# Optimization experiments

Measured on AMD Instinct MI355X. Metric: run time of the kernel, lower is better.

The kernel has to match this reference:

```python
import jax, jax.numpy as jnp
import numpy as np

D_MODEL = 1024
NUM_HEADS = 16
D_HEAD = D_MODEL // NUM_HEADS
NEG_INF = float(np.finfo(np.float32).min)


def setup_inputs() -> dict:
    key = jax.random.key(0)
    ks = jax.random.split(key, 6)
    B, S = 2, 2048
    q = jax.random.normal(ks[0], (B, S, D_MODEL), dtype=jnp.float32)
    k = jax.random.normal(ks[1], (B, S, D_MODEL), dtype=jnp.float32)
    v = jax.random.normal(ks[2], (B, S, D_MODEL), dtype=jnp.float32)
    # causal boolean mask: True = attend
    attn_mask = jnp.tril(jnp.ones((S, S), dtype=bool))
    # nn.Linear(d_model, d_model, bias=False) weights: [out, in]; y = x @ W.T
    init_scale = 1.0 / np.sqrt(D_MODEL)
    Wq = jax.random.uniform(ks[3], (D_MODEL, D_MODEL), jnp.float32, -init_scale, init_scale)
    Wk = jax.random.uniform(ks[4], (D_MODEL, D_MODEL), jnp.float32, -init_scale, init_scale)
    Wv = jax.random.uniform(ks[5], (D_MODEL, D_MODEL), jnp.float32, -init_scale, init_scale)
    return {"query": q, "key": k, "value": v, "Wq": Wq, "Wk": Wk, "Wv": Wv,
            "attn_mask": attn_mask}


def _split_heads(x):
    # [B, S, D_MODEL] -> [B, H, S, d_head]
    B, S, _ = x.shape
    return x.reshape(B, S, NUM_HEADS, D_HEAD).transpose(0, 2, 1, 3)


def reference(query, key, value, Wq, Wk, Wv, attn_mask):
    B, Sq, _ = query.shape
    Sk = key.shape[1]
    q = _split_heads(query @ Wq.T)   # [B, H, Sq, dh]
    k = _split_heads(key @ Wk.T)     # [B, H, Sk, dh]
    v = _split_heads(value @ Wv.T)   # [B, H, Sk, dh]
    scale = 1.0 / np.sqrt(D_HEAD)
    scores = jnp.einsum('bhqd,bhkd->bhqk', q, k) * scale  # [B, H, Sq, Sk]
    scores = jnp.where(attn_mask[None, None, :, :], scores, NEG_INF)
    attn_weights = jax.nn.softmax(scores, axis=-1)
    ctx = jnp.einsum('bhqk,bhkd->bhqd', attn_weights, v)   # [B, H, Sq, dh]
    context = ctx.transpose(0, 2, 1, 3).reshape(B, Sq, D_MODEL)
    return context, attn_weights
```

## Files before the change

kernel.cpp:

```cpp
#include <hip/hip_runtime.h>
#include <hip/hip_bf16.h>

#define B_ 2
#define H_ 16
#define S_ 2048
#define DH_ 64
#define DM_ 1024
#define BH_ (B_*H_)
#define CTX_ELEMS (B_*S_*DM_)
#define HEAD_ELEMS (S_*DH_)

typedef __attribute__((ext_vector_type(4))) float  f32x4;
typedef __attribute__((ext_vector_type(8))) short  short8;
typedef __attribute__((ext_vector_type(4))) unsigned short ush4;
typedef unsigned short u16;
typedef unsigned int u32;

__device__ __forceinline__ u16 f2bf(float f) {
  union { __hip_bfloat16 h; u16 u; } cv;
  cv.h = __float2bfloat16(f);
  return cv.u;
}
__device__ __forceinline__ float bf2f(u16 u) {
  union { unsigned int i; float f; } cv;
  cv.i = ((unsigned int)u) << 16;
  return cv.f;
}

__device__ __forceinline__ void gload_lds16(const u16* g, u16* l) {
  __builtin_amdgcn_global_load_lds(
      (const __attribute__((address_space(1))) u32*)g,
      (__attribute__((address_space(3))) u32*)l, 16, 0, 0);
}

__global__ __launch_bounds__(256) void convert_w(
    const float* __restrict__ w0, const float* __restrict__ w1,
    const float* __restrict__ w2, u16* __restrict__ o)
{
  const float* s = (blockIdx.y == 0) ? w0 : (blockIdx.y == 1) ? w1 : w2;
  u16* d = o + (size_t)blockIdx.y * (DM_ * DM_);
  const int i = (blockIdx.x * 256 + threadIdx.x) * 8;
  f32x4 a = *(const f32x4*)(s + i);
  f32x4 b = *(const f32x4*)(s + i + 4);
  short8 p;
#pragma unroll
  for (int j = 0; j < 4; ++j) { p[j] = (short)f2bf(a[j]); p[4 + j] = (short)f2bf(b[j]); }
  *(short8*)(d + i) = p;
}

__global__ __launch_bounds__(256) void proj_gemm(
    const float* __restrict__ X0, const float* __restrict__ X1, const float* __restrict__ X2,
    const u16* __restrict__ Wb,
    u16* __restrict__ O0, u16* __restrict__ O1, u16* __restrict__ O2)
{
  const float* X; u16* O;
  if (blockIdx.z == 0)      { X = X0; O = O0; }
  else if (blockIdx.z == 1) { X = X1; O = O1; }
  else                      { X = X2; O = O2; }
  const u16* W = Wb + (size_t)blockIdx.z * (DM_ * DM_);

  const int m0 = blockIdx.x * 128;
  const int n0 = blockIdx.y * 128;

  __shared__ u16 As[128][40];
  __shared__ u16 Bs[128 * 32];

  const int tid  = threadIdx.x;
  const int lane = tid & 63;
  const int w    = tid >> 6;
  const int wr   = w >> 1, wc = w & 1;
  const int l15  = lane & 15, l4 = lane >> 4;

  f32x4 acc[4][4];
#pragma unroll
  for (int i = 0; i < 4; ++i)
#pragma unroll
    for (int j = 0; j < 4; ++j) acc[i][j] = (f32x4){0.f, 0.f, 0.f, 0.f};

  const int srow  = tid >> 1;
  const int skoff = (tid & 1) * 16;

  const int brow0 = (w * 2) * 16 + (lane >> 2);
  const int bkoff = (lane & 3) * 8;

  for (int kb = 0; kb < DM_ / 32; ++kb) {
    const int k0 = kb * 32;
    gload_lds16(W + (size_t)(n0 + brow0) * DM_ + k0 + bkoff, &Bs[(w * 2) * 512]);
    gload_lds16(W + (size_t)(n0 + brow0 + 16) * DM_ + k0 + bkoff, &Bs[(w * 2 + 1) * 512]);
    {
      const float* ap = X + (size_t)(m0 + srow) * DM_ + k0 + skoff;
      float xa[16];
      *(f32x4*)&xa[0]  = *(const f32x4*)(ap);
      *(f32x4*)&xa[4]  = *(const f32x4*)(ap + 4);
      *(f32x4*)&xa[8]  = *(const f32x4*)(ap + 8);
      *(f32x4*)&xa[12] = *(const f32x4*)(ap + 12);
      short8 pa0, pa1;
#pragma unroll
      for (int j = 0; j < 8; ++j) {
        pa0[j] = (short)f2bf(xa[j]);
        pa1[j] = (short)f2bf(xa[8 + j]);
      }
      *(short8*)&As[srow][skoff]     = pa0;
      *(short8*)&As[srow][skoff + 8] = pa1;
    }
    __syncthreads();
    short8 af[4], bfr[4];
#pragma unroll
    for (int i = 0; i < 4; ++i)
      af[i] = *(const short8*)&As[wr * 64 + i * 16 + l15][l4 * 8];
#pragma unroll
    for (int j = 0; j < 4; ++j)
      bfr[j] = *(const short8*)&Bs[(wc * 64 + j * 16 + l15) * 32 + l4 * 8];
#pragma unroll
    for (int i = 0; i < 4; ++i)
#pragma unroll
      for (int j = 0; j < 4; ++j)
        acc[i][j] = __builtin_amdgcn_mfma_f32_16x16x32_bf16(af[i], bfr[j], acc[i][j], 0, 0, 0);
    __syncthreads();
  }

#pragma unroll
  for (int i = 0; i < 4; ++i) {
#pragma unroll
    for (int j = 0; j < 4; ++j) {
#pragma unroll
      for (int r = 0; r < 4; ++r) {
        const int grow = m0 + wr * 64 + i * 16 + l4 * 4 + r;
        const int gcol = n0 + wc * 64 + j * 16 + l15;
        const int b = grow >> 11, s = grow & (S_ - 1);
        const int h = gcol >> 6,  d = gcol & (DH_ - 1);
        O[(size_t)((b << 4) + h) * HEAD_ELEMS + (size_t)s * DH_ + d] = f2bf(acc[i][j][r]);
      }
    }
  }
}

__global__ __launch_bounds__(256) void transpose_v(const u16* __restrict__ vb,
                                                   u16* __restrict__ vt)
{
  __shared__ u16 T[64][72];
  const int bh = blockIdx.y;
  const int s0 = blockIdx.x * 64;
  const int tid = threadIdx.x;
  {
    const int sl = tid >> 2, dof = (tid & 3) * 16;
    const u16* src = vb + (size_t)bh * HEAD_ELEMS + (size_t)(s0 + sl) * DH_ + dof;
    *(short8*)&T[sl][dof]     = *(const short8*)(src);
    *(short8*)&T[sl][dof + 8] = *(const short8*)(src + 8);
  }
  __syncthreads();
  {
    const int dd = tid >> 2, sof = (tid & 3) * 16;
    u16* dst = vt + (size_t)bh * HEAD_ELEMS + (size_t)dd * S_ + s0 + sof;
    short8 t0, t1;
#pragma unroll
    for (int j = 0; j < 8; ++j) t0[j] = (short)T[sof + j][dd];
#pragma unroll
    for (int j = 0; j < 8; ++j) t1[j] = (short)T[sof + 8 + j][dd];
    *(short8*)(dst)     = t0;
    *(short8*)(dst + 8) = t1;
  }
}

#define PROW 2048
#define ATT_SMEM (16 * PROW * 2 + 16 * 4 + 64 * 4)

__global__ __launch_bounds__(256) void attn_kernel(
    const u16* __restrict__ qb, const u16* __restrict__ kb, const u16* __restrict__ vt,
    float* __restrict__ ctx, float* __restrict__ attnw)
{
  extern __shared__ u16 smem[];
  u16* P = smem;
  float* rinv    = (float*)(smem + 16 * PROW);
  float* partial = rinv + 16;

  const int bh = blockIdx.y;
  const int qt = 127 - blockIdx.x;
  const int tid = threadIdx.x;
  const int lane = tid & 63;
  const int w = tid >> 6;
  const int l15 = lane & 15, l4 = lane >> 4;

  const int NCC = ((qt * 16 + 16) + 127) >> 7;
  const int ncols = NCC << 7;

  const u16* Qb = qb + (size_t)bh * HEAD_ELEMS + (size_t)(qt * 16) * DH_;
  const u16* Kb = kb + (size_t)bh * HEAD_ELEMS;
  const u16* Vt = vt + (size_t)bh * HEAD_ELEMS;

  {
    short8 aQ0 = *(const short8*)(Qb + (size_t)l15 * DH_ + l4 * 8);
    short8 aQ1 = *(const short8*)(Qb + (size_t)l15 * DH_ + l4 * 8 + 32);
    const int qrow = l4 * 4;
    const int qabs = qt * 16 + qrow;
    float psum[4] = {0.f, 0.f, 0.f, 0.f};
    for (int ci = 0; ci < NCC; ++ci) {
      const int col0 = (ci << 7) + w * 32;
#pragma unroll
      for (int t = 0; t < 2; ++t) {
        const int ct = col0 + t * 16;
        const u16* kp = Kb + (size_t)(ct + l15) * DH_ + l4 * 8;
        short8 b0 = *(const short8*)(kp);
        short8 b1 = *(const short8*)(kp + 32);
        f32x4 a = (f32x4){0.f, 0.f, 0.f, 0.f};
        a = __builtin_amdgcn_mfma_f32_16x16x32_bf16(aQ0, b0, a, 0, 0, 0);
        a = __builtin_amdgcn_mfma_f32_16x16x32_bf16(aQ1, b1, a, 0, 0, 0);
        const int cg = ct + l15;
#pragma unroll
        for (int r = 0; r < 4; ++r) {
          const float e = (cg <= qabs + r) ? __expf(a[r] * 0.125f) : 0.f;
          psum[r] += e;
          const int row = qrow + r;
          P[(row << 11) + (cg ^ ((row & 7) << 3))] = f2bf(e);
        }
      }
    }
#pragma unroll
    for (int r = 0; r < 4; ++r) {
      float s = psum[r];
      s += __shfl_xor(s, 1);
      s += __shfl_xor(s, 2);
      s += __shfl_xor(s, 4);
      s += __shfl_xor(s, 8);
      if (l15 == 0) partial[w * 16 + qrow + r] = s;
    }
  }
  __syncthreads();
  if (tid < 16) {
    const float l = partial[tid] + partial[16 + tid] + partial[32 + tid] + partial[48 + tid];
    rinv[tid] = 1.0f / l;
  }
  __syncthreads();

  {
    const int row = tid >> 4, sub = tid & 15;
    const float inv = rinv[row];
    const int swz = (row & 7) << 3;
    const u16* prow = P + (row << 11);
    float* orow = attnw + (size_t)bh * ((size_t)S_ * S_) + (size_t)(qt * 16 + row) * S_;
    for (int c4 = sub * 4; c4 < S_; c4 += 64) {
      f32x4 o;
      if (c4 < ncols) {
        ush4 pv = *(const ush4*)(prow + (c4 ^ swz));
        o[0] = bf2f(pv[0]) * inv;
        o[1] = bf2f(pv[1]) * inv;
        o[2] = bf2f(pv[2]) * inv;
        o[3] = bf2f(pv[3]) * inv;
      } else {
        o = (f32x4){0.f, 0.f, 0.f, 0.f};
      }
      __builtin_nontemporal_store(o, (f32x4*)(orow + c4));
    }
  }

  {
    const int dq = w;
    f32x4 acc = (f32x4){0.f, 0.f, 0.f, 0.f};
    const u16* vp0 = Vt + (size_t)(dq * 16 + l15) * S_ + l4 * 8;
    const u16* prow = P + (l15 << 11);
    const int swz = (l15 & 7) << 3;
#pragma unroll 2
    for (int c = 0; c < ncols; c += 32) {
      short8 ap = *(const short8*)(prow + ((c + l4 * 8) ^ swz));
      short8 bv = *(const short8*)(vp0 + c);
      acc = __builtin_amdgcn_mfma_f32_16x16x32_bf16(ap, bv, acc, 0, 0, 0);
    }
    const int b = bh >> 4, h = bh & 15;
#pragma unroll
    for (int r = 0; r < 4; ++r) {
      const int rg = qt * 16 + l4 * 4 + r;
      const float inv = rinv[l4 * 4 + r];
      ctx[(size_t)(b * S_ + rg) * DM_ + h * 64 + dq * 16 + l15] = acc[r] * inv;
    }
  }
}

extern "C" void kernel_launch(void* const* d_in, const int* in_sizes, int n_in,
                              void* d_out, int out_size, void* d_ws, size_t ws_size,
                              hipStream_t stream) {
  const float* q  = (const float*)d_in[0];
  const float* k  = (const float*)d_in[1];
  const float* v  = (const float*)d_in[2];
  const float* Wq = (const float*)d_in[3];
  const float* Wk = (const float*)d_in[4];
  const float* Wv = (const float*)d_in[5];

  u16* wb = (u16*)d_ws;
  u16* qb = wb + (size_t)3 * DM_ * DM_;
  u16* kb = qb + (size_t)BH_ * HEAD_ELEMS;
  u16* vb = kb + (size_t)BH_ * HEAD_ELEMS;
  u16* vt = vb + (size_t)BH_ * HEAD_ELEMS;

  float* ctx   = (float*)d_out;
  float* attnw = ctx + CTX_ELEMS;

  hipFuncSetAttribute(reinterpret_cast<const void*>(attn_kernel),
                      hipFuncAttributeMaxDynamicSharedMemorySize, ATT_SMEM);

  convert_w<<<dim3(DM_ * DM_ / (256 * 8), 3), 256, 0, stream>>>(Wq, Wk, Wv, wb);
  proj_gemm<<<dim3(32, 8, 3), 256, 0, stream>>>(q, k, v, wb, qb, kb, vb);
  transpose_v<<<dim3(32, 32), 256, 0, stream>>>(vb, vt);
  attn_kernel<<<dim3(128, 32), 256, ATT_SMEM, stream>>>(qb, kb, vt, ctx, attnw);
}
```

Baseline: 252.8 us.

## Pre-convert activations to bf16, remap attention blocks, split MFMA accumulators

Activations q/k/v are converted to bf16 in a combined conversion kernel, using the attnw output buffer as scratch. The projection GEMM then loads both A and B tiles straight into LDS with global_load_lds instead of converting fp32 in registers, which cuts its global read volume. The attention kernel adds a block-index remap that interleaves heads and query tiles, and splits dependent MFMA chains into two accumulators. It also alternates the order of the attnw-write and PV phases between neighbouring blocks and uses nontemporal stores for ctx. The cost is an extra kernel pass that writes and rereads the bf16 activations.

After: 220.2 us. -12.9%, faster.

```diff
diff --git a/kernel.cpp b/kernel.cpp
--- a/kernel.cpp
+++ b/kernel.cpp
@@ -33,12 +33,23 @@
       (__attribute__((address_space(3))) u32*)l, 16, 0, 0);
 }
 
-__global__ __launch_bounds__(256) void convert_w(
-    const float* __restrict__ w0, const float* __restrict__ w1,
-    const float* __restrict__ w2, u16* __restrict__ o)
+__global__ __launch_bounds__(256) void convert_all(
+    const float* __restrict__ q, const float* __restrict__ k, const float* __restrict__ v,
+    const float* __restrict__ wq, const float* __restrict__ wk, const float* __restrict__ wv,
+    u16* __restrict__ xb, u16* __restrict__ wb)
 {
-  const float* s = (blockIdx.y == 0) ? w0 : (blockIdx.y == 1) ? w1 : w2;
-  u16* d = o + (size_t)blockIdx.y * (DM_ * DM_);
+  const int t = blockIdx.y;
+  const float* s; u16* d; int nblk;
+  if (t < 3) {
+    s = (t == 0) ? wq : (t == 1) ? wk : wv;
+    d = wb + (size_t)t * (DM_ * DM_);
+    nblk = 512;
+  } else {
+    s = (t == 3) ? q : (t == 4) ? k : v;
+    d = xb + (size_t)(t - 3) * ((size_t)B_ * S_ * DM_);
+    nblk = 2048;
+  }
+  if (blockIdx.x >= nblk) return;
   const int i = (blockIdx.x * 256 + threadIdx.x) * 8;
   f32x4 a = *(const f32x4*)(s + i);
   f32x4 b = *(const f32x4*)(s + i + 4);
@@ -49,20 +60,17 @@
 }
 
 __global__ __launch_bounds__(256) void proj_gemm(
-    const float* __restrict__ X0, const float* __restrict__ X1, const float* __restrict__ X2,
-    const u16* __restrict__ Wb,
+    const u16* __restrict__ Xb, const u16* __restrict__ Wb,
     u16* __restrict__ O0, u16* __restrict__ O1, u16* __restrict__ O2)
 {
-  const float* X; u16* O;
-  if (blockIdx.z == 0)      { X = X0; O = O0; }
-  else if (blockIdx.z == 1) { X = X1; O = O1; }
-  else                      { X = X2; O = O2; }
+  u16* O = (blockIdx.z == 0) ? O0 : (blockIdx.z == 1) ? O1 : O2;
+  const u16* A = Xb + (size_t)blockIdx.z * ((size_t)B_ * S_ * DM_);
   const u16* W = Wb + (size_t)blockIdx.z * (DM_ * DM_);
 
   const int m0 = blockIdx.x * 128;
   const int n0 = blockIdx.y * 128;
 
-  __shared__ u16 As[128][40];
+  __shared__ u16 As[128 * 32];
   __shared__ u16 Bs[128 * 32];
 
   const int tid  = threadIdx.x;
@@ -77,37 +85,25 @@
 #pragma unroll
     for (int j = 0; j < 4; ++j) acc[i][j] = (f32x4){0.f, 0.f, 0.f, 0.f};
 
-  const int srow  = tid >> 1;
-  const int skoff = (tid & 1) * 16;
-
-  const int brow0 = (w * 2) * 16 + (lane >> 2);
-  const int bkoff = (lane & 3) * 8;
+  const int srow = lane >> 2;
+  const int scol = (lane & 3) * 8;
+  const int ca = w * 2;
+  const u16* ga0 = A + (size_t)(m0 + ca * 16 + srow) * DM_ + scol;
+  const u16* ga1 = A + (size_t)(m0 + ca * 16 + 16 + srow) * DM_ + scol;
+  const u16* gb0 = W + (size_t)(n0 + ca * 16 + srow) * DM_ + scol;
+  const u16* gb1 = W + (size_t)(n0 + ca * 16 + 16 + srow) * DM_ + scol;
 
   for (int kb = 0; kb < DM_ / 32; ++kb) {
     const int k0 = kb * 32;
-    gload_lds16(W + (size_t)(n0 + brow0) * DM_ + k0 + bkoff, &Bs[(w * 2) * 512]);
-    gload_lds16(W + (size_t)(n0 + brow0 + 16) * DM_ + k0 + bkoff, &Bs[(w * 2 + 1) * 512]);
-    {
-      const float* ap = X + (size_t)(m0 + srow) * DM_ + k0 + skoff;
-      float xa[16];
-      *(f32x4*)&xa[0]  = *(const f32x4*)(ap);
-      *(f32x4*)&xa[4]  = *(const f32x4*)(ap + 4);
-      *(f32x4*)&xa[8]  = *(const f32x4*)(ap + 8);
-      *(f32x4*)&xa[12] = *(const f32x4*)(ap + 12);
-      short8 pa0, pa1;
-#pragma unroll
-      for (int j = 0; j < 8; ++j) {
-        pa0[j] = (short)f2bf(xa[j]);
-        pa1[j] = (short)f2bf(xa[8 + j]);
-      }
-      *(short8*)&As[srow][skoff]     = pa0;
-      *(short8*)&As[srow][skoff + 8] = pa1;
-    }
+    gload_lds16(ga0 + k0, &As[ca * 512]);
+    gload_lds16(ga1 + k0, &As[ca * 512 + 512]);
+    gload_lds16(gb0 + k0, &Bs[ca * 512]);
+    gload_lds16(gb1 + k0, &Bs[ca * 512 + 512]);
     __syncthreads();
     short8 af[4], bfr[4];
 #pragma unroll
     for (int i = 0; i < 4; ++i)
-      af[i] = *(const short8*)&As[wr * 64 + i * 16 + l15][l4 * 8];
+      af[i] = *(const short8*)&As[(wr * 64 + i * 16 + l15) * 32 + l4 * 8];
 #pragma unroll
     for (int j = 0; j < 4; ++j)
       bfr[j] = *(const short8*)&Bs[(wc * 64 + j * 16 + l15) * 32 + l4 * 8];
@@ -174,8 +170,12 @@
   float* rinv    = (float*)(smem + 16 * PROW);
   float* partial = rinv + 16;
 
-  const int bh = blockIdx.y;
-  const int qt = 127 - blockIdx.x;
+  const int lin = blockIdx.y * 128 + blockIdx.x;
+  const int nl  = (lin & 7) * 512 + (lin >> 3);
+  const int bh  = nl >> 7;
+  const int qtl = nl & 127;
+  const int qt  = 127 - qtl;
+
   const int tid = threadIdx.x;
   const int lane = tid & 63;
   const int w = tid >> 6;
@@ -202,9 +202,11 @@
         const u16* kp = Kb + (size_t)(ct + l15) * DH_ + l4 * 8;
         short8 b0 = *(const short8*)(kp);
         short8 b1 = *(const short8*)(kp + 32);
-        f32x4 a = (f32x4){0.f, 0.f, 0.f, 0.f};
-        a = __builtin_amdgcn_mfma_f32_16x16x32_bf16(aQ0, b0, a, 0, 0, 0);
-        a = __builtin_amdgcn_mfma_f32_16x16x32_bf16(aQ1, b1, a, 0, 0, 0);
+        f32x4 a0 = (f32x4){0.f, 0.f, 0.f, 0.f};
+        f32x4 a1 = (f32x4){0.f, 0.f, 0.f, 0.f};
+        a0 = __builtin_amdgcn_mfma_f32_16x16x32_bf16(aQ0, b0, a0, 0, 0, 0);
+        a1 = __builtin_amdgcn_mfma_f32_16x16x32_bf16(aQ1, b1, a1, 0, 0, 0);
+        const f32x4 a = a0 + a1;
         const int cg = ct + l15;
 #pragma unroll
         for (int r = 0; r < 4; ++r) {
@@ -232,7 +234,7 @@
   }
   __syncthreads();
 
-  {
+  auto phase2a = [&]() {
     const int row = tid >> 4, sub = tid & 15;
     const float inv = rinv[row];
     const int swz = (row & 7) << 3;
@@ -251,28 +253,36 @@
       }
       __builtin_nontemporal_store(o, (f32x4*)(orow + c4));
     }
-  }
-
-  {
+  };
+
+  auto phase2b = [&]() {
     const int dq = w;
-    f32x4 acc = (f32x4){0.f, 0.f, 0.f, 0.f};
+    f32x4 acc0 = (f32x4){0.f, 0.f, 0.f, 0.f};
+    f32x4 acc1 = (f32x4){0.f, 0.f, 0.f, 0.f};
     const u16* vp0 = Vt + (size_t)(dq * 16 + l15) * S_ + l4 * 8;
     const u16* prow = P + (l15 << 11);
     const int swz = (l15 & 7) << 3;
-#pragma unroll 2
-    for (int c = 0; c < ncols; c += 32) {
-      short8 ap = *(const short8*)(prow + ((c + l4 * 8) ^ swz));
-      short8 bv = *(const short8*)(vp0 + c);
-      acc = __builtin_amdgcn_mfma_f32_16x16x32_bf16(ap, bv, acc, 0, 0, 0);
-    }
+    for (int c = 0; c < ncols; c += 64) {
+      short8 ap0 = *(const short8*)(prow + ((c + l4 * 8) ^ swz));
+      short8 bv0 = *(const short8*)(vp0 + c);
+      acc0 = __builtin_amdgcn_mfma_f32_16x16x32_bf16(ap0, bv0, acc0, 0, 0, 0);
+      short8 ap1 = *(const short8*)(prow + ((c + 32 + l4 * 8) ^ swz));
+      short8 bv1 = *(const short8*)(vp0 + c + 32);
+      acc1 = __builtin_amdgcn_mfma_f32_16x16x32_bf16(ap1, bv1, acc1, 0, 0, 0);
+    }
+    const f32x4 acc = acc0 + acc1;
     const int b = bh >> 4, h = bh & 15;
 #pragma unroll
     for (int r = 0; r < 4; ++r) {
       const int rg = qt * 16 + l4 * 4 + r;
       const float inv = rinv[l4 * 4 + r];
-      ctx[(size_t)(b * S_ + rg) * DM_ + h * 64 + dq * 16 + l15] = acc[r] * inv;
-    }
-  }
+      __builtin_nontemporal_store(acc[r] * inv,
+          ctx + (size_t)(b * S_ + rg) * DM_ + h * 64 + dq * 16 + l15);
+    }
+  };
+
+  if (qtl & 1) { phase2b(); phase2a(); }
+  else         { phase2a(); phase2b(); }
 }
 
 extern "C" void kernel_launch(void* const* d_in, const int* in_sizes, int n_in,
@@ -285,20 +295,21 @@
   const float* Wk = (const float*)d_in[4];
   const float* Wv = (const float*)d_in[5];
 
+  float* ctx   = (float*)d_out;
+  float* attnw = ctx + CTX_ELEMS;
+
   u16* wb = (u16*)d_ws;
   u16* qb = wb + (size_t)3 * DM_ * DM_;
   u16* kb = qb + (size_t)BH_ * HEAD_ELEMS;
   u16* vb = kb + (size_t)BH_ * HEAD_ELEMS;
   u16* vt = vb + (size_t)BH_ * HEAD_ELEMS;
-
-  float* ctx   = (float*)d_out;
-  float* attnw = ctx + CTX_ELEMS;
+  u16* xb = (u16*)attnw;
 
   hipFuncSetAttribute(reinterpret_cast<const void*>(attn_kernel),
                       hipFuncAttributeMaxDynamicSharedMemorySize, ATT_SMEM);
 
-  convert_w<<<dim3(DM_ * DM_ / (256 * 8), 3), 256, 0, stream>>>(Wq, Wk, Wv, wb);
-  proj_gemm<<<dim3(32, 8, 3), 256, 0, stream>>>(q, k, v, wb, qb, kb, vb);
+  convert_all<<<dim3(2048, 6), 256, 0, stream>>>(q, k, v, Wq, Wk, Wv, xb, wb);
+  proj_gemm<<<dim3(32, 8, 3), 256, 0, stream>>>(xb, wb, qb, kb, vb);
   transpose_v<<<dim3(32, 32), 256, 0, stream>>>(vb, vt);
   attn_kernel<<<dim3(128, 32), 256, ATT_SMEM, stream>>>(qb, kb, vt, ctx, attnw);
 }
```
